# Optimization experiments

Measured on AMD Instinct MI355X. Metric: run time of the kernel, lower is better.

The kernel has to match this reference:

```python
import jax, jax.numpy as jnp
from jax import lax
import numpy as np

EPS = 1e-5
DN = ('NCHW', 'OIHW', 'NCHW')


def conv_s2(x, w):
    # Conv2d k=4 s=2 p=1, no bias
    return lax.conv_general_dilated(x, w, (2, 2), [(1, 1), (1, 1)], dimension_numbers=DN)


def deconv_s2(x, w):
    # ConvTranspose2d k=4 s=2 p=1; torch weight layout (in, out, kH, kW)
    w_ = jnp.flip(w, (2, 3)).transpose(1, 0, 2, 3)  # -> (out, in, kH, kW)
    return lax.conv_general_dilated(x, w_, (1, 1), [(2, 2), (2, 2)],
                                    lhs_dilation=(2, 2), dimension_numbers=DN)


def bn_train(x, gamma, beta):
    # BatchNorm2d in training mode: batch stats over (N, H, W), biased variance
    m = jnp.mean(x, axis=(0, 2, 3), keepdims=True)
    v = jnp.var(x, axis=(0, 2, 3), keepdims=True)
    g = gamma.reshape(1, -1, 1, 1)
    b = beta.reshape(1, -1, 1, 1)
    return (x - m) * jax.lax.rsqrt(v + EPS) * g + b


def lrelu(x):
    return jnp.where(x >= 0, x, 0.2 * x)


def setup_inputs() -> dict:
    key = jax.random.key(0)
    ks = jax.random.split(key, 32)
    nef = 64
    d = {}
    d['x'] = jax.random.normal(ks[0], (256, 3, 64, 64), dtype=jnp.float32)
    # encoder conv weights (O, I, 4, 4), init N(0, 0.02)
    d['w1'] = 0.02 * jax.random.normal(ks[1], (nef, 3, 4, 4), jnp.float32)
    d['w2'] = 0.02 * jax.random.normal(ks[2], (nef * 2, nef, 4, 4), jnp.float32)
    d['w3'] = 0.02 * jax.random.normal(ks[3], (nef * 4, nef * 2, 4, 4), jnp.float32)
    d['w4'] = 0.02 * jax.random.normal(ks[4], (nef * 8, nef * 4, 4, 4), jnp.float32)
    # bn params: weight ~ N(1, 0.02), bias = 0
    for i, c in enumerate([nef, nef * 2, nef * 4, nef * 8]):
        d[f'g{i+1}'] = 1.0 + 0.02 * jax.random.normal(ks[5 + i], (c,), jnp.float32)
        d[f'b{i+1}'] = jnp.zeros((c,), jnp.float32)
    # 512 channel-wise Linear(16,16): torch default init U(-1/4, 1/4)
    bound = 1.0 / 4.0
    d['cw_w'] = jax.random.uniform(ks[9], (512, 16, 16), jnp.float32, -bound, bound)
    d['cw_b'] = jax.random.uniform(ks[10], (512, 16), jnp.float32, -bound, bound)
    # decoder deconv weights in torch layout (in, out, 4, 4)
    d['dw1'] = 0.02 * jax.random.normal(ks[11], (nef * 8, nef * 4, 4, 4), jnp.float32)
    d['dw2'] = 0.02 * jax.random.normal(ks[12], (nef * 4, nef * 2, 4, 4), jnp.float32)
    d['dw3'] = 0.02 * jax.random.normal(ks[13], (nef * 2, nef, 4, 4), jnp.float32)
    d['dw4'] = 0.02 * jax.random.normal(ks[14], (nef, 3, 4, 4), jnp.float32)
    for i, c in enumerate([nef * 4, nef * 2, nef]):
        d[f'dg{i+1}'] = 1.0 + 0.02 * jax.random.normal(ks[15 + i], (c,), jnp.float32)
        d[f'db{i+1}'] = jnp.zeros((c,), jnp.float32)
    return d


def reference(x, w1, w2, w3, w4, g1, b1, g2, b2, g3, b3, g4, b4,
              cw_w, cw_b, dw1, dw2, dw3, dw4, dg1, db1, dg2, db2, dg3, db3):
    h = lrelu(bn_train(conv_s2(x, w1), g1, b1))
    h = lrelu(bn_train(conv_s2(h, w2), g2, b2))
    h = lrelu(bn_train(conv_s2(h, w3), g3, b3))
    h = lrelu(bn_train(conv_s2(h, w4), g4, b4))  # (B, 512, 4, 4)
    B, C, H, W = h.shape
    flat = h.reshape(B, C, H * W)  # (B, 512, 16)
    # per-channel Linear: y[b,c,t] = sum_s flat[b,c,s] * cw_w[c,t,s] + cw_b[c,t]
    flat = jnp.einsum('bcs,cts->bct', flat, cw_w) + cw_b[None, :, :]
    h = flat.reshape(B, C, H, W)
    h = jax.nn.relu(bn_train(deconv_s2(h, dw1), dg1, db1))
    h = jax.nn.relu(bn_train(deconv_s2(h, dw2), dg2, db2))
    h = jax.nn.relu(bn_train(deconv_s2(h, dw3), dg3, db3))
    return jnp.tanh(deconv_s2(h, dw4))
```

## Files before the change

### kernel.cpp

```cpp
#include <hip/hip_runtime.h>
#include <math.h>

typedef _Float16 f16;
typedef __attribute__((ext_vector_type(8))) _Float16 f16x8;
typedef __attribute__((ext_vector_type(16))) float f32x16;

union U64x2 { unsigned long long u[2]; f16x8 v; };
union Q16   { uint4 q; unsigned long long u[2]; };

constexpr int ilog2c(int x) { return x <= 1 ? 0 : 1 + ilog2c(x >> 1); }

__device__ __forceinline__ float fast_tanh(float x) {
    float e = __expf(2.f * x);
    return (e - 1.f) / (e + 1.f);
}

template<int CIN,int IH,int IW,int OH,int OW,int COUT,int COB,int SPT,int KS,
         int CO_FR,bool DEC>
__global__ __launch_bounds__(256,2) void mfma_conv(
    const f16* __restrict__ xin, const f16* __restrict__ wp,
    f16* __restrict__ out16, float* __restrict__ out32, size_t ps,
    float* __restrict__ psumF, float* __restrict__ psqF)
{
    constexpr int OHo  = DEC ? OH/2 : OH;
    constexpr int OWo  = DEC ? OW/2 : OW;
    constexpr int KTOT = CIN * (DEC ? 4 : 16);
    constexpr int CH   = (KTOT/64) / KS;
    constexpr int RPT  = CIN / 64;
    constexpr int RSH  = (RPT==1?0:RPT==2?1:RPT==4?2:3);
    constexpr int WSTR = CIN * 16;
    constexpr int TPR  = 256 / COB;
    constexpr int NU4  = 8 / TPR;
    constexpr int SPB  = OHo * OWo;
    constexpr int LSPB = ilog2c(SPB);
    constexpr int LOWo = ilog2c(OWo);

    __shared__ unsigned long long Xs[SPT*17];
    __shared__ unsigned long long Wls[COB*17];

    const int t   = threadIdx.x;
    const int bx  = blockIdx.x;
    const int cob = blockIdx.y;
    const int bz  = blockIdx.z;
    const int par = DEC ? (bz & 3) : 0;
    const int ks  = DEC ? (bz >> 2) : bz;
    const int poh = par >> 1, pw = par & 1;

    const int gsp_s = bx*SPT + t;
    const int img_s = gsp_s >> LSPB;
    const int r_s   = gsp_s & (SPB-1);
    const int oy_s  = r_s >> LOWo;
    const int ox_s  = r_s & (OWo-1);

    const int wco   = t / TPR;
    const int wpart = t % TPR;
    const f16* wbase = wp + (size_t)(cob*COB + wco)*WSTR + wpart*(64/TPR);

    const int wave = t >> 6, lane = t & 63, half = lane >> 5, l31 = lane & 31;
    const int co_w = (wave >> 1) * (CO_FR*32);
    const int sp_w = (wave & 1) * 128;

    f32x16 acc[CO_FR][4];
    #pragma unroll
    for (int i = 0; i < CO_FR; ++i)
        #pragma unroll
        for (int b = 0; b < 4; ++b)
            #pragma unroll
            for (int r = 0; r < 16; ++r) acc[i][b][r] = 0.f;

    uint4 xreg[8];
    uint4 wreg[NU4];

    auto issue = [&](int cc) {
        const int gc  = ks*CH + cc;
        const int tap = gc >> RSH;
        const int ci0 = (gc & (RPT-1)) << 6;
        int kh, kw, ih, iw;
        if (DEC) {
            const int t2h = tap >> 1, t2w = tap & 1;
            kh = (1-poh) + 2*t2h; kw = (1-pw) + 2*t2w;
            ih = oy_s + poh - t2h; iw = ox_s + pw - t2w;
        } else {
            kh = tap >> 2; kw = tap & 3;
            ih = 2*oy_s - 1 + kh; iw = 2*ox_s - 1 + kw;
        }
        const int woff = (kh*4 + kw)*CIN + ci0;
        const uint4* wsrc = (const uint4*)(wbase + woff);
        #pragma unroll
        for (int j = 0; j < NU4; ++j) wreg[j] = wsrc[j];
        const bool ok = (unsigned)ih < (unsigned)IH && (unsigned)iw < (unsigned)IW;
        if (ok) {
            const uint4* xsrc = (const uint4*)
                (xin + ((size_t)(img_s*IH + ih)*IW + iw)*CIN + ci0);
            #pragma unroll
            for (int j = 0; j < 8; ++j) xreg[j] = xsrc[j];
        } else {
            #pragma unroll
            for (int j = 0; j < 8; ++j) xreg[j] = uint4{0u,0u,0u,0u};
        }
    };

    issue(0);

    for (int cc = 0; cc < CH; ++cc) {
        if (cc) __syncthreads();

        #pragma unroll
        for (int j = 0; j < NU4; ++j) {
            Q16 v; v.q = wreg[j];
            const int u0 = wco*17 + wpart*(NU4*2) + j*2;
            Wls[u0]   = v.u[0];
            Wls[u0+1] = v.u[1];
        }
        {
            const int u0 = t*17;
            #pragma unroll
            for (int j = 0; j < 8; ++j) {
                Q16 v; v.q = xreg[j];
                Xs[u0 + j*2]   = v.u[0];
                Xs[u0 + j*2+1] = v.u[1];
            }
        }

        if (cc + 1 < CH) issue(cc + 1);

        asm volatile("s_waitcnt lgkmcnt(0)" ::: "memory");
        __builtin_amdgcn_sched_barrier(0);
        __builtin_amdgcn_s_barrier();
        __builtin_amdgcn_sched_barrier(0);

        #pragma unroll
        for (int kk = 0; kk < 4; ++kk) {
            const int uo = kk*4 + 2*half;
            f16x8 wf[CO_FR], xf[4];
            #pragma unroll
            for (int i = 0; i < CO_FR; ++i) {
                U64x2 u; const int rw = (co_w + i*32 + l31)*17 + uo;
                u.u[0] = Wls[rw]; u.u[1] = Wls[rw+1]; wf[i] = u.v;
            }
            #pragma unroll
            for (int b = 0; b < 4; ++b) {
                U64x2 u; const int rx = (sp_w + b*32 + l31)*17 + uo;
                u.u[0] = Xs[rx]; u.u[1] = Xs[rx+1]; xf[b] = u.v;
            }
            #pragma unroll
            for (int i = 0; i < CO_FR; ++i)
                #pragma unroll
                for (int b = 0; b < 4; ++b)
                    acc[i][b] = __builtin_amdgcn_mfma_f32_32x32x16_f16(
                        xf[b], wf[i], acc[i][b], 0, 0, 0);
        }
    }

    #pragma unroll
    for (int b = 0; b < 4; ++b) {
        #pragma unroll
        for (int q = 0; q < 4; ++q) {
            #pragma unroll
            for (int r2 = 0; r2 < 4; ++r2) {
                const int sp_loc = sp_w + b*32 + q*8 + 4*half + r2;
                const int gsp    = bx*SPT + sp_loc;
                size_t base;
                if (DEC) {
                    const int img = gsp >> LSPB;
                    const int r   = gsp & (SPB-1);
                    const int oh  = 2*(r >> LOWo) + poh;
                    const int ow  = 2*(r & (OWo-1)) + pw;
                    base = ((size_t)(img*OH + oh)*OW + ow)*COUT + cob*COB;
                } else {
                    base = (size_t)gsp*COUT + cob*COB;
                }
                #pragma unroll
                for (int i = 0; i < CO_FR; ++i) {
                    const int co_l = co_w + i*32 + l31;
                    const float v  = acc[i][b][q*4 + r2];
                    if (KS == 1) out16[base + co_l] = (_Float16)v;
                    else         out32[(size_t)ks*ps + base + co_l] = v;
                }
            }
        }
    }

    if (KS == 1 && psumF != nullptr) {
        #pragma unroll
        for (int i = 0; i < CO_FR; ++i) {
            float s = 0.f, q = 0.f;
            #pragma unroll
            for (int b = 0; b < 4; ++b)
                #pragma unroll
                for (int r = 0; r < 16; ++r) {
                    const float v = acc[i][b][r];
                    s += v; q += v * v;
                }
            s += __shfl_down(s, 32);
            q += __shfl_down(q, 32);
            if (half == 0) {
                const int co = cob*COB + co_w + i*32 + l31;
                atomicAdd(psumF + co, s);
                atomicAdd(psqF + co, q);
            }
        }
    }
}

__global__ __launch_bounds__(256,2) void conv1_mfma(
    const f16* __restrict__ xp, const f16* __restrict__ wp,
    f16* __restrict__ out, float* __restrict__ psumF, float* __restrict__ psqF)
{
    __shared__ unsigned long long Xs[256*17];
    __shared__ unsigned long long Wls[64*17];
    const int t = threadIdx.x, bx = blockIdx.x;

    {
        const int r = t >> 2, part = t & 3;
        const uint4* src = (const uint4*)(wp + r*64 + part*16);
        Q16 v0; v0.q = src[0];
        Q16 v1; v1.q = src[1];
        const int u0 = r*17 + part*4;
        Wls[u0]   = v0.u[0]; Wls[u0+1] = v0.u[1];
        Wls[u0+2] = v1.u[0]; Wls[u0+3] = v1.u[1];
    }
    {
        const int gsp = bx*256 + t;
        const int n = gsp >> 10, r = gsp & 1023;
        const int oy = r >> 5, ox = r & 31;
        const int ih0 = 2*oy - 1, iw0 = 2*ox - 1;
        const int u0 = t*17;
        #pragma unroll
        for (int tap = 0; tap < 16; ++tap) {
            const int ih = ih0 + (tap >> 2), iw = iw0 + (tap & 3);
            unsigned long long v = 0ull;
            if ((unsigned)ih < 64u && (unsigned)iw < 64u)
                v = *(const unsigned long long*)(xp + (((size_t)n*64 + ih)*64 + iw)*4);
            Xs[u0 + tap] = v;
        }
    }
    __syncthreads();

    const int wave = t >> 6, lane = t & 63, half = lane >> 5, l31 = lane & 31;
    const int co_w = (wave >> 1) * 32;
    const int sp_w = (wave & 1) * 128;

    f32x16 acc[4];
    #pragma unroll
    for (int b = 0; b < 4; ++b)
        #pragma unroll
        for (int r = 0; r < 16; ++r) acc[b][r] = 0.f;

    #pragma unroll
    for (int kk = 0; kk < 4; ++kk) {
        const int uo = kk*4 + 2*half;
        U64x2 uw; const int rw = (co_w + l31)*17 + uo;
        uw.u[0] = Wls[rw]; uw.u[1] = Wls[rw+1];
        #pragma unroll
        for (int b = 0; b < 4; ++b) {
            U64x2 ux; const int rx = (sp_w + b*32 + l31)*17 + uo;
            ux.u[0] = Xs[rx]; ux.u[1] = Xs[rx+1];
            acc[b] = __builtin_amdgcn_mfma_f32_32x32x16_f16(
                ux.v, uw.v, acc[b], 0, 0, 0);
        }
    }
    #pragma unroll
    for (int b = 0; b < 4; ++b)
        #pragma unroll
        for (int q = 0; q < 4; ++q)
            #pragma unroll
            for (int r2 = 0; r2 < 4; ++r2) {
                const int sp_loc = sp_w + b*32 + q*8 + 4*half + r2;
                out[(size_t)(bx*256 + sp_loc)*64 + co_w + l31] =
                    (_Float16)acc[b][q*4 + r2];
            }

    float s = 0.f, q = 0.f;
    #pragma unroll
    for (int b = 0; b < 4; ++b)
        #pragma unroll
        for (int r = 0; r < 16; ++r) {
            const float v = acc[b][r];
            s += v; q += v * v;
        }
    s += __shfl_down(s, 32);
    q += __shfl_down(q, 32);
    if (half == 0) {
        const int co = co_w + l31;
        atomicAdd(psumF + co, s);
        atomicAdd(psqF + co, q);
    }
}

__global__ __launch_bounds__(256,2) void deconv4_mfma(
    const f16* __restrict__ xin, const f16* __restrict__ wp,
    float* __restrict__ out)
{
    __shared__ unsigned long long Xs[256*17];
    __shared__ unsigned long long Wls[32*17];

    const int t   = threadIdx.x;
    const int bx  = blockIdx.x;
    const int par = blockIdx.y;
    const int poh = par >> 1, pw = par & 1;

    const int gsp_s = bx*256 + t;
    const int img_s = gsp_s >> 10;
    const int r_s   = gsp_s & 1023;
    const int oy_s  = r_s >> 5;
    const int ox_s  = r_s & 31;

    const int wco   = t >> 3;
    const int wpart = t & 7;

    const int wave = t >> 6, lane = t & 63, half = lane >> 5, l31 = lane & 31;
    const int sp_w = wave * 64;

    f32x16 acc[2];
    #pragma unroll
    for (int b = 0; b < 2; ++b)
        #pragma unroll
        for (int r = 0; r < 16; ++r) acc[b][r] = 0.f;

    uint4 xreg[8];
    uint4 wreg1;

    auto issue4 = [&](int cc) {
        const int t2h = cc >> 1, t2w = cc & 1;
        const int kh = (1-poh) + 2*t2h, kw = (1-pw) + 2*t2w;
        const int ih = oy_s + poh - t2h, iw = ox_s + pw - t2w;
        wreg1 = *(const uint4*)(wp + wco*1024 + (kh*4 + kw)*64 + wpart*8);
        const bool ok = (unsigned)ih < 32u && (unsigned)iw < 32u;
        if (ok) {
            const uint4* src = (const uint4*)
                (xin + ((size_t)(img_s*32 + ih)*32 + iw)*64);
            #pragma unroll
            for (int j = 0; j < 8; ++j) xreg[j] = src[j];
        } else {
            #pragma unroll
            for (int j = 0; j < 8; ++j) xreg[j] = uint4{0u,0u,0u,0u};
        }
    };

    issue4(0);

    for (int cc = 0; cc < 4; ++cc) {
        if (cc) __syncthreads();
        {
            Q16 v; v.q = wreg1;
            const int u0 = wco*17 + wpart*2;
            Wls[u0] = v.u[0]; Wls[u0+1] = v.u[1];
        }
        {
            const int u0 = t*17;
            #pragma unroll
            for (int j = 0; j < 8; ++j) {
                Q16 v; v.q = xreg[j];
                Xs[u0 + j*2]   = v.u[0];
                Xs[u0 + j*2+1] = v.u[1];
            }
        }
        if (cc + 1 < 4) issue4(cc + 1);
        asm volatile("s_waitcnt lgkmcnt(0)" ::: "memory");
        __builtin_amdgcn_sched_barrier(0);
        __builtin_amdgcn_s_barrier();
        __builtin_amdgcn_sched_barrier(0);

        #pragma unroll
        for (int kk = 0; kk < 4; ++kk) {
            const int uo = kk*4 + 2*half;
            U64x2 uw; const int rw = l31*17 + uo;
            uw.u[0] = Wls[rw]; uw.u[1] = Wls[rw+1];
            #pragma unroll
            for (int b = 0; b < 2; ++b) {
                U64x2 ux; const int rx = (sp_w + b*32 + l31)*17 + uo;
                ux.u[0] = Xs[rx]; ux.u[1] = Xs[rx+1];
                acc[b] = __builtin_amdgcn_mfma_f32_32x32x16_f16(
                    uw.v, ux.v, acc[b], 0, 0, 0);
            }
        }
    }

    if (half == 0) {
        #pragma unroll
        for (int b = 0; b < 2; ++b) {
            const int gsp = bx*256 + sp_w + b*32 + l31;
            const int img = gsp >> 10;
            const int r   = gsp & 1023;
            const int oh  = 2*(r >> 5) + poh;
            const int ow  = 2*(r & 31) + pw;
            #pragma unroll
            for (int co = 0; co < 3; ++co)
                out[(((size_t)img*3 + co)*64 + oh)*64 + ow] =
                    fast_tanh(acc[b][co]);
        }
    }
}

__global__ __launch_bounds__(256) void prep_x(
    const float* __restrict__ x, f16* __restrict__ xp)
{
    const int i = blockIdx.x*256 + threadIdx.x;
    const int n = i >> 12, p = i & 4095;
    const float* b = x + (size_t)n*12288 + p;
    union { _Float16 h[4]; unsigned long long u; } o;
    o.h[0] = (_Float16)b[0];
    o.h[1] = (_Float16)b[4096];
    o.h[2] = (_Float16)b[8192];
    o.h[3] = (_Float16)0.f;
    *(unsigned long long*)(xp + (size_t)i*4) = o.u;
}

__global__ __launch_bounds__(256) void prep_w1(
    const float* __restrict__ w1, f16* __restrict__ wp)
{
    const int e = blockIdx.x*256 + threadIdx.x;
    const int co = e >> 6, k = e & 63, tap = k >> 2, ci = k & 3;
    const float v = (ci < 3) ? w1[(co*3 + ci)*16 + tap] : 0.f;
    wp[e] = (_Float16)v;
}

__global__ __launch_bounds__(256) void prep_w4(
    const float* __restrict__ dw4, f16* __restrict__ wp)
{
    const int e = blockIdx.x*256 + threadIdx.x;
    const int co = e >> 10, r = e & 1023, khw = r >> 6, ci = r & 63;
    const float v = (co < 3) ? dw4[(ci*3 + co)*16 + khw] : 0.f;
    wp[e] = (_Float16)v;
}

__global__ __launch_bounds__(256) void prep_w(
    const float* __restrict__ w2, const float* __restrict__ w3,
    const float* __restrict__ w4, const float* __restrict__ dw1,
    const float* __restrict__ dw2, const float* __restrict__ dw3,
    f16* __restrict__ dst)
{
    const int e = blockIdx.x*256 + threadIdx.x;
    float v;
    if (e < 131072) {
        int co = e >> 10, r = e & 1023, khw = r >> 6, ci = r & 63;
        v = w2[(co*64 + ci)*16 + khw];
    } else if (e < 655360) {
        int l = e - 131072;
        int co = l >> 11, r = l & 2047, khw = r >> 7, ci = r & 127;
        v = w3[(co*128 + ci)*16 + khw];
    } else if (e < 2752512) {
        int l = e - 655360;
        int co = l >> 12, r = l & 4095, khw = r >> 8, ci = r & 255;
        v = w4[(co*256 + ci)*16 + khw];
    } else if (e < 4849664) {
        int l = e - 2752512;
        int co = l >> 13, r = l & 8191, khw = r >> 9, ci = r & 511;
        v = dw1[(ci*256 + co)*16 + khw];
    } else if (e < 5373952) {
        int l = e - 4849664;
        int co = l >> 12, r = l & 4095, khw = r >> 8, ci = r & 255;
        v = dw2[(ci*128 + co)*16 + khw];
    } else {
        int l = e - 5373952;
        int co = l >> 11, r = l & 2047, khw = r >> 7, ci = r & 127;
        v = dw3[(ci*64 + co)*16 + khw];
    }
    dst[e] = (_Float16)v;
}

template<typename T, int P>
__global__ __launch_bounds__(256) void bn_partial(
    const T* __restrict__ x, size_t ps, float* __restrict__ psum,
    float* __restrict__ psq, int C, int rowsPerS, int S)
{
    const int s = blockIdx.x;
    const int c = (blockIdx.y << 6) + (threadIdx.x & 63);
    float a = 0.f, q = 0.f;
    const int rEnd = (s + 1) * rowsPerS;
    for (int r = s*rowsPerS + (threadIdx.x >> 6); r < rEnd; r += 4) {
        float v = 0.f;
        #pragma unroll
        for (int p = 0; p < P; ++p)
            v += (float)x[p*ps + (size_t)r * C + c];
        a += v; q += v * v;
    }
    __shared__ float ls[256], lq[256];
    ls[threadIdx.x] = a; lq[threadIdx.x] = q;
    __syncthreads();
    if (threadIdx.x < 64) {
        a = ls[threadIdx.x] + ls[threadIdx.x+64] + ls[threadIdx.x+128] + ls[threadIdx.x+192];
        q = lq[threadIdx.x] + lq[threadIdx.x+64] + lq[threadIdx.x+128] + lq[threadIdx.x+192];
        psum[c * S + s] = a; psq[c * S + s] = q;
    }
}

__global__ __launch_bounds__(256) void bn_finalize(
    const float* __restrict__ psum, const float* __restrict__ psq,
    const float* __restrict__ gamma, const float* __restrict__ beta,
    float* __restrict__ scale, float* __restrict__ shift,
    int C, int S, float inv_count)
{
    int c = blockIdx.x * 256 + threadIdx.x;
    if (c >= C) return;
    float s = 0.f, q = 0.f;
    for (int i = 0; i < S; ++i) { s += psum[c*S + i]; q += psq[c*S + i]; }
    float m   = s * inv_count;
    float var = q * inv_count - m * m;
    var = var < 0.f ? 0.f : var;
    float sc = gamma[c] * rsqrtf(var + 1e-5f);
    scale[c] = sc;
    shift[c] = beta[c] - m * sc;
}

__global__ __launch_bounds__(256) void bn_act16f(
    f16* __restrict__ x, const float* __restrict__ psum, const float* __restrict__ psq,
    const float* __restrict__ gamma, const float* __restrict__ beta,
    int Cmask, float inv_count, float slope)
{
    const size_t i8 = ((size_t)blockIdx.x*256 + threadIdx.x) * 8;
    union { uint4 u; _Float16 h[8]; } a;
    a.u = *(const uint4*)(x + i8);
    const int c0 = (int)(i8 & (size_t)Cmask);
    #pragma unroll
    for (int j = 0; j < 8; ++j) {
        const int c = c0 + j;
        float m   = psum[c] * inv_count;
        float var = psq[c] * inv_count - m * m;
        var = var < 0.f ? 0.f : var;
        float sc = gamma[c] * rsqrtf(var + 1e-5f);
        float sh = beta[c] - m * sc;
        float v = (float)a.h[j] * sc + sh;
        a.h[j] = (_Float16)(v >= 0.f ? v : slope * v);
    }
    *(uint4*)(x + i8) = a.u;
}

template<int P>
__global__ __launch_bounds__(256) void bn_act32(
    const float* __restrict__ x, size_t ps, f16* __restrict__ y,
    const float* __restrict__ sc, const float* __restrict__ sh,
    int Cmask, float slope)
{
    const size_t i8 = ((size_t)blockIdx.x*256 + threadIdx.x) * 8;
    float xv[8] = {0,0,0,0,0,0,0,0};
    #pragma unroll
    for (int p = 0; p < P; ++p) {
        float4 v0 = *(const float4*)(x + p*ps + i8);
        float4 v1 = *(const float4*)(x + p*ps + i8 + 4);
        xv[0]+=v0.x; xv[1]+=v0.y; xv[2]+=v0.z; xv[3]+=v0.w;
        xv[4]+=v1.x; xv[5]+=v1.y; xv[6]+=v1.z; xv[7]+=v1.w;
    }
    union { uint4 u; _Float16 h[8]; } a;
    const int c0 = (int)(i8 & (size_t)Cmask);
    #pragma unroll
    for (int j = 0; j < 8; ++j) {
        float v = xv[j] * sc[c0+j] + sh[c0+j];
        a.h[j] = (_Float16)(v >= 0.f ? v : slope * v);
    }
    *(uint4*)(y + i8) = a.u;
}

__global__ __launch_bounds__(256) void chanlin16(
    const f16* __restrict__ in, const float* __restrict__ w,
    const float* __restrict__ bias, f16* __restrict__ out)
{
    const int i = blockIdx.x*256 + threadIdx.x;
    const int c  = i & 511;
    const int bt = i >> 9;
    const int b  = bt >> 4, tt = bt & 15;
    const f16* src = in + ((size_t)b*16)*512 + c;
    const float* wr = w + ((size_t)c*16 + tt)*16;
    float acc = bias[c*16 + tt];
    #pragma unroll
    for (int s = 0; s < 16; ++s)
        acc = fmaf((float)src[s*512], wr[s], acc);
    out[i] = (_Float16)acc;
}

extern "C" void kernel_launch(void* const* d_in, const int* in_sizes, int n_in,
                              void* d_out, int out_size, void* d_ws, size_t ws_size,
                              hipStream_t stream)
{
    const float* x   = (const float*)d_in[0];
    const float* w1  = (const float*)d_in[1];
    const float* w2  = (const float*)d_in[2];
    const float* w3  = (const float*)d_in[3];
    const float* w4  = (const float*)d_in[4];
    const float* g1  = (const float*)d_in[5];
    const float* b1  = (const float*)d_in[6];
    const float* g2  = (const float*)d_in[7];
    const float* b2  = (const float*)d_in[8];
    const float* g3  = (const float*)d_in[9];
    const float* b3  = (const float*)d_in[10];
    const float* g4  = (const float*)d_in[11];
    const float* b4  = (const float*)d_in[12];
    const float* cww = (const float*)d_in[13];
    const float* cwb = (const float*)d_in[14];
    const float* dw1 = (const float*)d_in[15];
    const float* dw2 = (const float*)d_in[16];
    const float* dw3 = (const float*)d_in[17];
    const float* dw4 = (const float*)d_in[18];
    const float* dg1 = (const float*)d_in[19];
    const float* db1 = (const float*)d_in[20];
    const float* dg2 = (const float*)d_in[21];
    const float* db2 = (const float*)d_in[22];
    const float* dg3 = (const float*)d_in[23];
    const float* db3 = (const float*)d_in[24];

    char* WS = (char*)d_ws;
    float* psum  = (float*)WS;
    float* psq   = (float*)(WS + 65536);
    float* scale = (float*)(WS + 131072);
    float* shift = (float*)(WS + 133120);
    float* fst   = (float*)(WS + 196608);
    f16* slotA   = (f16*)(WS + 262144);
    f16* slotB   = (f16*)(WS + 262144 + 33554432);
    f16* wprep   = (f16*)(WS + 84148224);
    f16* wprep1  = wprep + 5505024;
    f16* wprep4  = wprep1 + 4096;

    f16*   A_hi  = slotA + 8388608;
    float* pB    = (float*)slotB;
    f16*   xpack = slotA;

    float* fs0 = fst;          float* fs1 = fst + 1024;
    float* fs2 = fst + 2048;   float* fs4 = fst + 4096;
    float* fs5 = fst + 5120;   float* fs6 = fst + 6144;

    hipMemsetAsync(fst, 0, 28672, stream);
    prep_w<<<21504, 256, 0, stream>>>(w2, w3, w4, dw1, dw2, dw3, wprep);
    prep_w1<<<16, 256, 0, stream>>>(w1, wprep1);
    prep_w4<<<128, 256, 0, stream>>>(dw4, wprep4);
    prep_x<<<4096, 256, 0, stream>>>(x, xpack);

    conv1_mfma<<<1024, 256, 0, stream>>>(xpack, wprep1, slotB, fs0, fs0 + 512);
    bn_act16f<<<8192, 256, 0, stream>>>(slotB, fs0, fs0 + 512, g1, b1, 63, 1.f/262144.f, 0.2f);

    mfma_conv<64,32,32,16,16,128, 128,256,1,2,false><<<dim3(256,1,1), 256, 0, stream>>>(
        slotB, wprep, slotA, nullptr, 0, fs1, fs1 + 512);
    bn_act16f<<<4096, 256, 0, stream>>>(slotA, fs1, fs1 + 512, g2, b2, 127, 1.f/65536.f, 0.2f);

    mfma_conv<128,16,16,8,8,256, 64,256,1,1,false><<<dim3(64,4,1), 256, 0, stream>>>(
        slotA, wprep + 131072, A_hi, nullptr, 0, fs2, fs2 + 512);
    bn_act16f<<<2048, 256, 0, stream>>>(A_hi, fs2, fs2 + 512, g3, b3, 255, 1.f/16384.f, 0.2f);

    mfma_conv<256,8,8,4,4,512, 128,256,4,2,false><<<dim3(16,4,4), 256, 0, stream>>>(
        A_hi, wprep + 655360, nullptr, pB, (size_t)2097152, nullptr, nullptr);
    bn_partial<float,4><<<dim3(32,8), 256, 0, stream>>>(pB, (size_t)2097152, psum, psq, 512, 128, 32);
    bn_finalize<<<2, 256, 0, stream>>>(psum, psq, g4, b4, scale, shift, 512, 32, 1.f/4096.f);
    bn_act32<4><<<1024, 256, 0, stream>>>(pB, (size_t)2097152, slotA, scale, shift, 511, 0.2f);

    chanlin16<<<8192, 256, 0, stream>>>(slotA, cww, cwb, slotB);

    mfma_conv<512,4,4,8,8,256, 64,256,1,1,true><<<dim3(16,4,4), 256, 0, stream>>>(
        slotB, wprep + 2752512, A_hi, nullptr, 0, fs4, fs4 + 512);
    bn_act16f<<<2048, 256, 0, stream>>>(A_hi, fs4, fs4 + 512, dg1, db1, 255, 1.f/16384.f, 0.f);

    mfma_conv<256,8,8,16,16,128, 128,256,1,2,true><<<dim3(64,1,4), 256, 0, stream>>>(
        A_hi, wprep + 4849664, slotB, nullptr, 0, fs5, fs5 + 512);
    bn_act16f<<<4096, 256, 0, stream>>>(slotB, fs5, fs5 + 512, dg2, db2, 127, 1.f/65536.f, 0.f);

    mfma_conv<128,16,16,32,32,64, 64,256,1,1,true><<<dim3(256,1,4), 256, 0, stream>>>(
        slotB, wprep + 5373952, slotA, nullptr, 0, fs6, fs6 + 512);
    bn_act16f<<<8192, 256, 0, stream>>>(slotA, fs6, fs6 + 512, dg3, db3, 63, 1.f/262144.f, 0.f);

    deconv4_mfma<<<dim3(1024,4), 256, 0, stream>>>(slotA, wprep4, (float*)d_out);
}
```

Measured before the change: 613.7 us.

## Load weight fragments directly from global into registers and double-buffer input LDS

Weight MFMA fragments are now read by each lane straight from global memory into registers, dropping the weight shared-memory staging. The input tile in LDS is double-buffered, which lets the leading __syncthreads per chunk be removed. The aim is to cut LDS traffic and one barrier per K-chunk. In exchange it doubles the input LDS footprint, adds register pressure from the weight fragments, and makes weight loads exposed with no prefetch because they are issued in the same iteration they are used.

```diff
diff --git a/kernel.cpp b/kernel.cpp
--- a/kernel.cpp
+++ b/kernel.cpp
@@ -7,6 +7,7 @@
 
 union U64x2 { unsigned long long u[2]; f16x8 v; };
 union Q16   { uint4 q; unsigned long long u[2]; };
+union UW    { uint4 q; f16x8 v; };
 
 constexpr int ilog2c(int x) { return x <= 1 ? 0 : 1 + ilog2c(x >> 1); }
 
@@ -29,14 +30,11 @@
     constexpr int RPT  = CIN / 64;
     constexpr int RSH  = (RPT==1?0:RPT==2?1:RPT==4?2:3);
     constexpr int WSTR = CIN * 16;
-    constexpr int TPR  = 256 / COB;
-    constexpr int NU4  = 8 / TPR;
     constexpr int SPB  = OHo * OWo;
     constexpr int LSPB = ilog2c(SPB);
     constexpr int LOWo = ilog2c(OWo);
 
-    __shared__ unsigned long long Xs[SPT*17];
-    __shared__ unsigned long long Wls[COB*17];
+    __shared__ unsigned long long Xs[2][SPT*17];
 
     const int t   = threadIdx.x;
     const int bx  = blockIdx.x;
@@ -52,14 +50,15 @@
     const int oy_s  = r_s >> LOWo;
     const int ox_s  = r_s & (OWo-1);
 
-    const int wco   = t / TPR;
-    const int wpart = t % TPR;
-    const f16* wbase = wp + (size_t)(cob*COB + wco)*WSTR + wpart*(64/TPR);
-
     const int wave = t >> 6, lane = t & 63, half = lane >> 5, l31 = lane & 31;
     const int co_w = (wave >> 1) * (CO_FR*32);
     const int sp_w = (wave & 1) * 128;
 
+    const f16* wrow[CO_FR];
+    #pragma unroll
+    for (int i = 0; i < CO_FR; ++i)
+        wrow[i] = wp + (size_t)(cob*COB + co_w + i*32 + l31)*WSTR + 8*half;
+
     f32x16 acc[CO_FR][4];
     #pragma unroll
     for (int i = 0; i < CO_FR; ++i)
@@ -69,25 +68,19 @@
             for (int r = 0; r < 16; ++r) acc[i][b][r] = 0.f;
 
     uint4 xreg[8];
-    uint4 wreg[NU4];
-
-    auto issue = [&](int cc) {
+    uint4 wfrag[CO_FR][4];
+
+    auto issueX = [&](int cc) {
         const int gc  = ks*CH + cc;
         const int tap = gc >> RSH;
         const int ci0 = (gc & (RPT-1)) << 6;
-        int kh, kw, ih, iw;
+        int ih, iw;
         if (DEC) {
             const int t2h = tap >> 1, t2w = tap & 1;
-            kh = (1-poh) + 2*t2h; kw = (1-pw) + 2*t2w;
             ih = oy_s + poh - t2h; iw = ox_s + pw - t2w;
         } else {
-            kh = tap >> 2; kw = tap & 3;
-            ih = 2*oy_s - 1 + kh; iw = 2*ox_s - 1 + kw;
-        }
-        const int woff = (kh*4 + kw)*CIN + ci0;
-        const uint4* wsrc = (const uint4*)(wbase + woff);
-        #pragma unroll
-        for (int j = 0; j < NU4; ++j) wreg[j] = wsrc[j];
+            ih = 2*oy_s - 1 + (tap >> 2); iw = 2*ox_s - 1 + (tap & 3);
+        }
         const bool ok = (unsigned)ih < (unsigned)IH && (unsigned)iw < (unsigned)IW;
         if (ok) {
             const uint4* xsrc = (const uint4*)
@@ -100,29 +93,42 @@
         }
     };
 
-    issue(0);
+    auto loadW = [&](int cc) {
+        const int gc  = ks*CH + cc;
+        const int tap = gc >> RSH;
+        const int ci0 = (gc & (RPT-1)) << 6;
+        int kh, kw;
+        if (DEC) {
+            kh = (1-poh) + 2*(tap >> 1); kw = (1-pw) + 2*(tap & 1);
+        } else {
+            kh = tap >> 2; kw = tap & 3;
+        }
+        const int woff = (kh*4 + kw)*CIN + ci0;
+        #pragma unroll
+        for (int i = 0; i < CO_FR; ++i)
+            #pragma unroll
+            for (int kk = 0; kk < 4; ++kk)
+                wfrag[i][kk] = *(const uint4*)(wrow[i] + woff + kk*16);
+    };
+
+    issueX(0);
 
     for (int cc = 0; cc < CH; ++cc) {
-        if (cc) __syncthreads();
-
-        #pragma unroll
-        for (int j = 0; j < NU4; ++j) {
-            Q16 v; v.q = wreg[j];
-            const int u0 = wco*17 + wpart*(NU4*2) + j*2;
-            Wls[u0]   = v.u[0];
-            Wls[u0+1] = v.u[1];
-        }
+        const int buf = cc & 1;
+
+        loadW(cc);
+
         {
             const int u0 = t*17;
             #pragma unroll
             for (int j = 0; j < 8; ++j) {
                 Q16 v; v.q = xreg[j];
-                Xs[u0 + j*2]   = v.u[0];
-                Xs[u0 + j*2+1] = v.u[1];
-            }
-        }
-
-        if (cc + 1 < CH) issue(cc + 1);
+                Xs[buf][u0 + j*2]   = v.u[0];
+                Xs[buf][u0 + j*2+1] = v.u[1];
+            }
+        }
+
+        if (cc + 1 < CH) issueX(cc + 1);
 
         asm volatile("s_waitcnt lgkmcnt(0)" ::: "memory");
         __builtin_amdgcn_sched_barrier(0);
@@ -135,13 +141,12 @@
             f16x8 wf[CO_FR], xf[4];
             #pragma unroll
             for (int i = 0; i < CO_FR; ++i) {
-                U64x2 u; const int rw = (co_w + i*32 + l31)*17 + uo;
-                u.u[0] = Wls[rw]; u.u[1] = Wls[rw+1]; wf[i] = u.v;
+                UW u; u.q = wfrag[i][kk]; wf[i] = u.v;
             }
             #pragma unroll
             for (int b = 0; b < 4; ++b) {
                 U64x2 u; const int rx = (sp_w + b*32 + l31)*17 + uo;
-                u.u[0] = Xs[rx]; u.u[1] = Xs[rx+1]; xf[b] = u.v;
+                u.u[0] = Xs[buf][rx]; u.u[1] = Xs[buf][rx+1]; xf[b] = u.v;
             }
             #pragma unroll
             for (int i = 0; i < CO_FR; ++i)
@@ -292,8 +297,7 @@
     const f16* __restrict__ xin, const f16* __restrict__ wp,
     float* __restrict__ out)
 {
-    __shared__ unsigned long long Xs[256*17];
-    __shared__ unsigned long long Wls[32*17];
+    __shared__ unsigned long long Xs[2][256*17];
 
     const int t   = threadIdx.x;
     const int bx  = blockIdx.x;
@@ -306,12 +310,11 @@
     const int oy_s  = r_s >> 5;
     const int ox_s  = r_s & 31;
 
-    const int wco   = t >> 3;
-    const int wpart = t & 7;
-
     const int wave = t >> 6, lane = t & 63, half = lane >> 5, l31 = lane & 31;
     const int sp_w = wave * 64;
 
+    const f16* wrow = wp + l31*1024 + 8*half;
+
     f32x16 acc[2];
     #pragma unroll
     for (int b = 0; b < 2; ++b)
@@ -319,13 +322,11 @@
         for (int r = 0; r < 16; ++r) acc[b][r] = 0.f;
 
     uint4 xreg[8];
-    uint4 wreg1;
-
-    auto issue4 = [&](int cc) {
+    uint4 wfrag[4];
+
+    auto issueX4 = [&](int cc) {
         const int t2h = cc >> 1, t2w = cc & 1;
-        const int kh = (1-poh) + 2*t2h, kw = (1-pw) + 2*t2w;
         const int ih = oy_s + poh - t2h, iw = ox_s + pw - t2w;
-        wreg1 = *(const uint4*)(wp + wco*1024 + (kh*4 + kw)*64 + wpart*8);
         const bool ok = (unsigned)ih < 32u && (unsigned)iw < 32u;
         if (ok) {
             const uint4* src = (const uint4*)
@@ -338,25 +339,30 @@
         }
     };
 
-    issue4(0);
+    auto loadW4 = [&](int cc) {
+        const int t2h = cc >> 1, t2w = cc & 1;
+        const int kh = (1-poh) + 2*t2h, kw = (1-pw) + 2*t2w;
+        const int woff = (kh*4 + kw)*64;
+        #pragma unroll
+        for (int kk = 0; kk < 4; ++kk)
+            wfrag[kk] = *(const uint4*)(wrow + woff + kk*16);
+    };
+
+    issueX4(0);
 
     for (int cc = 0; cc < 4; ++cc) {
-        if (cc) __syncthreads();
-        {
-            Q16 v; v.q = wreg1;
-            const int u0 = wco*17 + wpart*2;
-            Wls[u0] = v.u[0]; Wls[u0+1] = v.u[1];
-        }
+        const int buf = cc & 1;
+        loadW4(cc);
         {
             const int u0 = t*17;
             #pragma unroll
             for (int j = 0; j < 8; ++j) {
                 Q16 v; v.q = xreg[j];
-                Xs[u0 + j*2]   = v.u[0];
-                Xs[u0 + j*2+1] = v.u[1];
-            }
-        }
-        if (cc + 1 < 4) issue4(cc + 1);
+                Xs[buf][u0 + j*2]   = v.u[0];
+                Xs[buf][u0 + j*2+1] = v.u[1];
+            }
+        }
+        if (cc + 1 < 4) issueX4(cc + 1);
         asm volatile("s_waitcnt lgkmcnt(0)" ::: "memory");
         __builtin_amdgcn_sched_barrier(0);
         __builtin_amdgcn_s_barrier();
@@ -365,12 +371,11 @@
         #pragma unroll
         for (int kk = 0; kk < 4; ++kk) {
             const int uo = kk*4 + 2*half;
-            U64x2 uw; const int rw = l31*17 + uo;
-            uw.u[0] = Wls[rw]; uw.u[1] = Wls[rw+1];
+            UW uw; uw.q = wfrag[kk];
             #pragma unroll
             for (int b = 0; b < 2; ++b) {
                 U64x2 ux; const int rx = (sp_w + b*32 + l31)*17 + uo;
-                ux.u[0] = Xs[rx]; ux.u[1] = Xs[rx+1];
+                ux.u[0] = Xs[buf][rx]; ux.u[1] = Xs[buf][rx+1];
                 acc[b] = __builtin_amdgcn_mfma_f32_32x32x16_f16(
                     uw.v, ux.v, acc[b], 0, 0, 0);
             }
```

After: 692.6 us. 1.13x slower.

## Coalesce activation loads across threads, add XCD block swizzle, pair-unroll K loop

Applied to the files above, without the earlier changes.

Global activation loads are restructured so that 8 consecutive threads read one spatial position's 64-channel row, each taking a 16-byte slice, rather than each thread reading a full 128-byte row alone. This makes accesses coalesced across neighbouring lanes. Block indices are remapped so that consecutive tiles land on the same XCD, which is meant to improve L2 locality. The K loop is unrolled in pairs with ping-pong weight registers. The trade-off is more per-load address arithmetic and bounds checks, and higher register pressure.

```diff
diff --git a/kernel.cpp b/kernel.cpp
--- a/kernel.cpp
+++ b/kernel.cpp
@@ -13,6 +13,10 @@
 __device__ __forceinline__ float fast_tanh(float x) {
     float e = __expf(2.f * x);
     return (e - 1.f) / (e + 1.f);
+}
+
+__device__ __forceinline__ int xcd_swz(int bx, int n) {
+    return ((n & 7) == 0) ? ((bx & 7) * (n >> 3) + (bx >> 3)) : bx;
 }
 
 template<int CIN,int IH,int IW,int OH,int OW,int COUT,int COB,int SPT,int KS,
@@ -34,23 +38,22 @@
     constexpr int SPB  = OHo * OWo;
     constexpr int LSPB = ilog2c(SPB);
     constexpr int LOWo = ilog2c(OWo);
+    static_assert(CH % 2 == 0, "pair-unrolled K loop needs even CH");
 
     __shared__ unsigned long long Xs[SPT*17];
     __shared__ unsigned long long Wls[COB*17];
 
     const int t   = threadIdx.x;
-    const int bx  = blockIdx.x;
+    const int bx  = xcd_swz(blockIdx.x, gridDim.x);
     const int cob = blockIdx.y;
     const int bz  = blockIdx.z;
     const int par = DEC ? (bz & 3) : 0;
     const int ks  = DEC ? (bz >> 2) : bz;
     const int poh = par >> 1, pw = par & 1;
 
-    const int gsp_s = bx*SPT + t;
-    const int img_s = gsp_s >> LSPB;
-    const int r_s   = gsp_s & (SPB-1);
-    const int oy_s  = r_s >> LOWo;
-    const int ox_s  = r_s & (OWo-1);
+    const int rloc  = t >> 3;
+    const int sub8  = (t & 7) * 8;
+    const int gbase = bx*SPT + rloc;
 
     const int wco   = t / TPR;
     const int wpart = t % TPR;
@@ -69,60 +72,66 @@
             for (int r = 0; r < 16; ++r) acc[i][b][r] = 0.f;
 
     uint4 xreg[8];
-    uint4 wreg[NU4];
-
-    auto issue = [&](int cc) {
+    uint4 wregA[NU4], wregB[NU4];
+
+    auto issueX = [&](int cc) {
         const int gc  = ks*CH + cc;
         const int tap = gc >> RSH;
         const int ci0 = (gc & (RPT-1)) << 6;
-        int kh, kw, ih, iw;
-        if (DEC) {
-            const int t2h = tap >> 1, t2w = tap & 1;
-            kh = (1-poh) + 2*t2h; kw = (1-pw) + 2*t2w;
-            ih = oy_s + poh - t2h; iw = ox_s + pw - t2w;
-        } else {
-            kh = tap >> 2; kw = tap & 3;
-            ih = 2*oy_s - 1 + kh; iw = 2*ox_s - 1 + kw;
-        }
+        int dh, dw;
+        if (DEC) { dh = poh - (tap >> 1); dw = pw - (tap & 1); }
+        else     { dh = (tap >> 2) - 1;   dw = (tap & 3) - 1; }
+        #pragma unroll
+        for (int j = 0; j < 8; ++j) {
+            const int gsp = gbase + j*32;
+            const int img = gsp >> LSPB;
+            const int rr  = gsp & (SPB-1);
+            const int oy  = rr >> LOWo;
+            const int ox  = rr & (OWo-1);
+            const int ih  = (DEC ? oy : 2*oy) + dh;
+            const int iw  = (DEC ? ox : 2*ox) + dw;
+            const bool ok = (unsigned)ih < (unsigned)IH && (unsigned)iw < (unsigned)IW;
+            if (ok) {
+                xreg[j] = *(const uint4*)
+                    (xin + ((size_t)(img*IH + ih)*IW + iw)*CIN + ci0 + sub8);
+            } else {
+                xreg[j] = uint4{0u,0u,0u,0u};
+            }
+        }
+    };
+
+    auto issueW = [&](int cc, uint4 (&wr)[NU4]) {
+        const int gc  = ks*CH + cc;
+        const int tap = gc >> RSH;
+        const int ci0 = (gc & (RPT-1)) << 6;
+        int kh, kw;
+        if (DEC) { kh = (1-poh) + 2*(tap >> 1); kw = (1-pw) + 2*(tap & 1); }
+        else     { kh = tap >> 2;               kw = tap & 3; }
         const int woff = (kh*4 + kw)*CIN + ci0;
         const uint4* wsrc = (const uint4*)(wbase + woff);
         #pragma unroll
-        for (int j = 0; j < NU4; ++j) wreg[j] = wsrc[j];
-        const bool ok = (unsigned)ih < (unsigned)IH && (unsigned)iw < (unsigned)IW;
-        if (ok) {
-            const uint4* xsrc = (const uint4*)
-                (xin + ((size_t)(img_s*IH + ih)*IW + iw)*CIN + ci0);
-            #pragma unroll
-            for (int j = 0; j < 8; ++j) xreg[j] = xsrc[j];
-        } else {
-            #pragma unroll
-            for (int j = 0; j < 8; ++j) xreg[j] = uint4{0u,0u,0u,0u};
-        }
+        for (int j = 0; j < NU4; ++j) wr[j] = wsrc[j];
     };
 
-    issue(0);
-
-    for (int cc = 0; cc < CH; ++cc) {
+    auto body = [&](int cc, uint4 (&wcur)[NU4], uint4 (&wnext)[NU4], bool more) {
         if (cc) __syncthreads();
 
         #pragma unroll
+        for (int j = 0; j < 8; ++j) {
+            Q16 v; v.q = xreg[j];
+            const int u0 = (rloc + j*32)*17 + (sub8 >> 2);
+            Xs[u0]   = v.u[0];
+            Xs[u0+1] = v.u[1];
+        }
+        #pragma unroll
         for (int j = 0; j < NU4; ++j) {
-            Q16 v; v.q = wreg[j];
+            Q16 v; v.q = wcur[j];
             const int u0 = wco*17 + wpart*(NU4*2) + j*2;
             Wls[u0]   = v.u[0];
             Wls[u0+1] = v.u[1];
         }
-        {
-            const int u0 = t*17;
-            #pragma unroll
-            for (int j = 0; j < 8; ++j) {
-                Q16 v; v.q = xreg[j];
-                Xs[u0 + j*2]   = v.u[0];
-                Xs[u0 + j*2+1] = v.u[1];
-            }
-        }
-
-        if (cc + 1 < CH) issue(cc + 1);
+
+        if (more) { issueX(cc + 1); issueW(cc + 1, wnext); }
 
         asm volatile("s_waitcnt lgkmcnt(0)" ::: "memory");
         __builtin_amdgcn_sched_barrier(0);
@@ -150,6 +159,13 @@
                     acc[i][b] = __builtin_amdgcn_mfma_f32_32x32x16_f16(
                         xf[b], wf[i], acc[i][b], 0, 0, 0);
         }
+    };
+
+    issueX(0);
+    issueW(0, wregA);
+    for (int cc = 0; cc < CH; cc += 2) {
+        body(cc,   wregA, wregB, true);
+        body(cc+1, wregB, wregA, cc+2 < CH);
     }
 
     #pragma unroll
@@ -209,7 +225,8 @@
 {
     __shared__ unsigned long long Xs[256*17];
     __shared__ unsigned long long Wls[64*17];
-    const int t = threadIdx.x, bx = blockIdx.x;
+    const int t = threadIdx.x;
+    const int bx = xcd_swz(blockIdx.x, gridDim.x);
 
     {
         const int r = t >> 2, part = t & 3;
@@ -296,15 +313,13 @@
     __shared__ unsigned long long Wls[32*17];
 
     const int t   = threadIdx.x;
-    const int bx  = blockIdx.x;
+    const int bx  = xcd_swz(blockIdx.x, gridDim.x);
     const int par = blockIdx.y;
     const int poh = par >> 1, pw = par & 1;
 
-    const int gsp_s = bx*256 + t;
-    const int img_s = gsp_s >> 10;
-    const int r_s   = gsp_s & 1023;
-    const int oy_s  = r_s >> 5;
-    const int ox_s  = r_s & 31;
+    const int rloc  = t >> 3;
+    const int sub8  = (t & 7) * 8;
+    const int gbase = bx*256 + rloc;
 
     const int wco   = t >> 3;
     const int wpart = t & 7;
@@ -319,44 +334,48 @@
         for (int r = 0; r < 16; ++r) acc[b][r] = 0.f;
 
     uint4 xreg[8];
-    uint4 wreg1;
-
-    auto issue4 = [&](int cc) {
-        const int t2h = cc >> 1, t2w = cc & 1;
-        const int kh = (1-poh) + 2*t2h, kw = (1-pw) + 2*t2w;
-        const int ih = oy_s + poh - t2h, iw = ox_s + pw - t2w;
-        wreg1 = *(const uint4*)(wp + wco*1024 + (kh*4 + kw)*64 + wpart*8);
-        const bool ok = (unsigned)ih < 32u && (unsigned)iw < 32u;
-        if (ok) {
-            const uint4* src = (const uint4*)
-                (xin + ((size_t)(img_s*32 + ih)*32 + iw)*64);
-            #pragma unroll
-            for (int j = 0; j < 8; ++j) xreg[j] = src[j];
-        } else {
-            #pragma unroll
-            for (int j = 0; j < 8; ++j) xreg[j] = uint4{0u,0u,0u,0u};
+    uint4 wregA, wregB;
+
+    auto issueX4 = [&](int cc) {
+        const int dh = poh - (cc >> 1), dw = pw - (cc & 1);
+        #pragma unroll
+        for (int j = 0; j < 8; ++j) {
+            const int gsp = gbase + j*32;
+            const int img = gsp >> 10;
+            const int rr  = gsp & 1023;
+            const int oy  = rr >> 5;
+            const int ox  = rr & 31;
+            const int ih  = oy + dh, iw = ox + dw;
+            const bool ok = (unsigned)ih < 32u && (unsigned)iw < 32u;
+            if (ok) {
+                xreg[j] = *(const uint4*)
+                    (xin + ((size_t)(img*32 + ih)*32 + iw)*64 + sub8);
+            } else {
+                xreg[j] = uint4{0u,0u,0u,0u};
+            }
         }
     };
 
-    issue4(0);
-
-    for (int cc = 0; cc < 4; ++cc) {
+    auto issueW4 = [&](int cc, uint4& wr) {
+        const int kh = (1-poh) + 2*(cc >> 1), kw = (1-pw) + 2*(cc & 1);
+        wr = *(const uint4*)(wp + wco*1024 + (kh*4 + kw)*64 + wpart*8);
+    };
+
+    auto body4 = [&](int cc, uint4& wcur, uint4& wnext, bool more) {
         if (cc) __syncthreads();
+        #pragma unroll
+        for (int j = 0; j < 8; ++j) {
+            Q16 v; v.q = xreg[j];
+            const int u0 = (rloc + j*32)*17 + (sub8 >> 2);
+            Xs[u0]   = v.u[0];
+            Xs[u0+1] = v.u[1];
+        }
         {
-            Q16 v; v.q = wreg1;
+            Q16 v; v.q = wcur;
             const int u0 = wco*17 + wpart*2;
             Wls[u0] = v.u[0]; Wls[u0+1] = v.u[1];
         }
-        {
-            const int u0 = t*17;
-            #pragma unroll
-            for (int j = 0; j < 8; ++j) {
-                Q16 v; v.q = xreg[j];
-                Xs[u0 + j*2]   = v.u[0];
-                Xs[u0 + j*2+1] = v.u[1];
-            }
-        }
-        if (cc + 1 < 4) issue4(cc + 1);
+        if (more) { issueX4(cc + 1); issueW4(cc + 1, wnext); }
         asm volatile("s_waitcnt lgkmcnt(0)" ::: "memory");
         __builtin_amdgcn_sched_barrier(0);
         __builtin_amdgcn_s_barrier();
@@ -375,7 +394,14 @@
                     uw.v, ux.v, acc[b], 0, 0, 0);
             }
         }
-    }
+    };
+
+    issueX4(0);
+    issueW4(0, wregA);
+    body4(0, wregA, wregB, true);
+    body4(1, wregB, wregA, true);
+    body4(2, wregA, wregB, true);
+    body4(3, wregB, wregA, false);
 
     if (half == 0) {
         #pragma unroll
```

After: 689.1 us. 12.3% more time.

## XOR-swizzle LDS tiles, raise occupancy, and halve output-channel tiles

Applied to the files above, without the earlier changes.

Replaces the padded stride-17 LDS layout with a stride-16 layout that XOR-swizzles the 16-byte chunks by row, so each ds read stays 16-byte aligned and avoids bank conflicts. It raises the launch-bounds minimum blocks from 2 to 4 in the MFMA conv kernels. Three conv launches move from COB=128 with CO_FR=2 to COB=64 with CO_FR=1, doubling the grid. More blocks and fewer accumulators per block should help latency hiding, but each block reuses its loaded input tile across fewer output channels, and the tighter register budget could cause spills.

```diff
diff --git a/kernel.cpp b/kernel.cpp
--- a/kernel.cpp
+++ b/kernel.cpp
@@ -17,7 +17,7 @@
 
 template<int CIN,int IH,int IW,int OH,int OW,int COUT,int COB,int SPT,int KS,
          int CO_FR,bool DEC>
-__global__ __launch_bounds__(256,2) void mfma_conv(
+__global__ __launch_bounds__(256,4) void mfma_conv(
     const f16* __restrict__ xin, const f16* __restrict__ wp,
     f16* __restrict__ out16, float* __restrict__ out32, size_t ps,
     float* __restrict__ psumF, float* __restrict__ psqF)
@@ -35,8 +35,8 @@
     constexpr int LSPB = ilog2c(SPB);
     constexpr int LOWo = ilog2c(OWo);
 
-    __shared__ unsigned long long Xs[SPT*17];
-    __shared__ unsigned long long Wls[COB*17];
+    __shared__ unsigned long long Xs[SPT*16];
+    __shared__ unsigned long long Wls[COB*16];
 
     const int t   = threadIdx.x;
     const int bx  = blockIdx.x;
@@ -59,6 +59,7 @@
     const int wave = t >> 6, lane = t & 63, half = lane >> 5, l31 = lane & 31;
     const int co_w = (wave >> 1) * (CO_FR*32);
     const int sp_w = (wave & 1) * 128;
+    const int swz  = l31 & 7;
 
     f32x16 acc[CO_FR][4];
     #pragma unroll
@@ -108,17 +109,18 @@
         #pragma unroll
         for (int j = 0; j < NU4; ++j) {
             Q16 v; v.q = wreg[j];
-            const int u0 = wco*17 + wpart*(NU4*2) + j*2;
+            const int sl = wpart*NU4 + j;
+            const int u0 = wco*16 + ((sl ^ (wco & 7)) << 1);
             Wls[u0]   = v.u[0];
             Wls[u0+1] = v.u[1];
         }
         {
-            const int u0 = t*17;
             #pragma unroll
             for (int j = 0; j < 8; ++j) {
                 Q16 v; v.q = xreg[j];
-                Xs[u0 + j*2]   = v.u[0];
-                Xs[u0 + j*2+1] = v.u[1];
+                const int u0 = t*16 + ((j ^ (t & 7)) << 1);
+                Xs[u0]   = v.u[0];
+                Xs[u0+1] = v.u[1];
             }
         }
 
@@ -131,16 +133,16 @@
 
         #pragma unroll
         for (int kk = 0; kk < 4; ++kk) {
-            const int uo = kk*4 + 2*half;
+            const int so = ((kk*2 + half) ^ swz) << 1;
             f16x8 wf[CO_FR], xf[4];
             #pragma unroll
             for (int i = 0; i < CO_FR; ++i) {
-                U64x2 u; const int rw = (co_w + i*32 + l31)*17 + uo;
+                U64x2 u; const int rw = (co_w + i*32 + l31)*16 + so;
                 u.u[0] = Wls[rw]; u.u[1] = Wls[rw+1]; wf[i] = u.v;
             }
             #pragma unroll
             for (int b = 0; b < 4; ++b) {
-                U64x2 u; const int rx = (sp_w + b*32 + l31)*17 + uo;
+                U64x2 u; const int rx = (sp_w + b*32 + l31)*16 + so;
                 u.u[0] = Xs[rx]; u.u[1] = Xs[rx+1]; xf[b] = u.v;
             }
             #pragma unroll
@@ -203,12 +205,12 @@
     }
 }
 
-__global__ __launch_bounds__(256,2) void conv1_mfma(
+__global__ __launch_bounds__(256,4) void conv1_mfma(
     const f16* __restrict__ xp, const f16* __restrict__ wp,
     f16* __restrict__ out, float* __restrict__ psumF, float* __restrict__ psqF)
 {
-    __shared__ unsigned long long Xs[256*17];
-    __shared__ unsigned long long Wls[64*17];
+    __shared__ unsigned long long Xs[256*16];
+    __shared__ unsigned long long Wls[64*16];
     const int t = threadIdx.x, bx = blockIdx.x;
 
     {
@@ -216,23 +218,24 @@
         const uint4* src = (const uint4*)(wp + r*64 + part*16);
         Q16 v0; v0.q = src[0];
         Q16 v1; v1.q = src[1];
-        const int u0 = r*17 + part*4;
-        Wls[u0]   = v0.u[0]; Wls[u0+1] = v0.u[1];
-        Wls[u0+2] = v1.u[0]; Wls[u0+3] = v1.u[1];
+        const int a0 = r*16 + (((part*2)   ^ (r & 7)) << 1);
+        const int a1 = r*16 + (((part*2+1) ^ (r & 7)) << 1);
+        Wls[a0]   = v0.u[0]; Wls[a0+1] = v0.u[1];
+        Wls[a1]   = v1.u[0]; Wls[a1+1] = v1.u[1];
     }
     {
         const int gsp = bx*256 + t;
         const int n = gsp >> 10, r = gsp & 1023;
         const int oy = r >> 5, ox = r & 31;
         const int ih0 = 2*oy - 1, iw0 = 2*ox - 1;
-        const int u0 = t*17;
         #pragma unroll
         for (int tap = 0; tap < 16; ++tap) {
             const int ih = ih0 + (tap >> 2), iw = iw0 + (tap & 3);
             unsigned long long v = 0ull;
             if ((unsigned)ih < 64u && (unsigned)iw < 64u)
                 v = *(const unsigned long long*)(xp + (((size_t)n*64 + ih)*64 + iw)*4);
-            Xs[u0 + tap] = v;
+            const int u = t*16 + (((tap >> 1) ^ (t & 7)) << 1) + (tap & 1);
+            Xs[u] = v;
         }
     }
     __syncthreads();
@@ -240,6 +243,7 @@
     const int wave = t >> 6, lane = t & 63, half = lane >> 5, l31 = lane & 31;
     const int co_w = (wave >> 1) * 32;
     const int sp_w = (wave & 1) * 128;
+    const int swz  = l31 & 7;
 
     f32x16 acc[4];
     #pragma unroll
@@ -249,12 +253,12 @@
 
     #pragma unroll
     for (int kk = 0; kk < 4; ++kk) {
-        const int uo = kk*4 + 2*half;
-        U64x2 uw; const int rw = (co_w + l31)*17 + uo;
+        const int so = ((kk*2 + half) ^ swz) << 1;
+        U64x2 uw; const int rw = (co_w + l31)*16 + so;
         uw.u[0] = Wls[rw]; uw.u[1] = Wls[rw+1];
         #pragma unroll
         for (int b = 0; b < 4; ++b) {
-            U64x2 ux; const int rx = (sp_w + b*32 + l31)*17 + uo;
+            U64x2 ux; const int rx = (sp_w + b*32 + l31)*16 + so;
             ux.u[0] = Xs[rx]; ux.u[1] = Xs[rx+1];
             acc[b] = __builtin_amdgcn_mfma_f32_32x32x16_f16(
                 ux.v, uw.v, acc[b], 0, 0, 0);
@@ -288,12 +292,12 @@
     }
 }
 
-__global__ __launch_bounds__(256,2) void deconv4_mfma(
+__global__ __launch_bounds__(256,4) void deconv4_mfma(
     const f16* __restrict__ xin, const f16* __restrict__ wp,
     float* __restrict__ out)
 {
-    __shared__ unsigned long long Xs[256*17];
-    __shared__ unsigned long long Wls[32*17];
+    __shared__ unsigned long long Xs[256*16];
+    __shared__ unsigned long long Wls[32*16];
 
     const int t   = threadIdx.x;
     const int bx  = blockIdx.x;
@@ -311,6 +315,7 @@
 
     const int wave = t >> 6, lane = t & 63, half = lane >> 5, l31 = lane & 31;
     const int sp_w = wave * 64;
+    const int swz  = l31 & 7;
 
     f32x16 acc[2];
     #pragma unroll
@@ -344,16 +349,16 @@
         if (cc) __syncthreads();
         {
             Q16 v; v.q = wreg1;
-            const int u0 = wco*17 + wpart*2;
+            const int u0 = wco*16 + ((wpart ^ (wco & 7)) << 1);
             Wls[u0] = v.u[0]; Wls[u0+1] = v.u[1];
         }
         {
-            const int u0 = t*17;
             #pragma unroll
             for (int j = 0; j < 8; ++j) {
                 Q16 v; v.q = xreg[j];
-                Xs[u0 + j*2]   = v.u[0];
-                Xs[u0 + j*2+1] = v.u[1];
+                const int u0 = t*16 + ((j ^ (t & 7)) << 1);
+                Xs[u0]   = v.u[0];
+                Xs[u0+1] = v.u[1];
             }
         }
         if (cc + 1 < 4) issue4(cc + 1);
@@ -364,12 +369,12 @@
 
         #pragma unroll
         for (int kk = 0; kk < 4; ++kk) {
-            const int uo = kk*4 + 2*half;
-            U64x2 uw; const int rw = l31*17 + uo;
+            const int so = ((kk*2 + half) ^ swz) << 1;
+            U64x2 uw; const int rw = l31*16 + so;
             uw.u[0] = Wls[rw]; uw.u[1] = Wls[rw+1];
             #pragma unroll
             for (int b = 0; b < 2; ++b) {
-                U64x2 ux; const int rx = (sp_w + b*32 + l31)*17 + uo;
+                U64x2 ux; const int rx = (sp_w + b*32 + l31)*16 + so;
                 ux.u[0] = Xs[rx]; ux.u[1] = Xs[rx+1];
                 acc[b] = __builtin_amdgcn_mfma_f32_32x32x16_f16(
                     uw.v, ux.v, acc[b], 0, 0, 0);
@@ -628,7 +633,7 @@
     conv1_mfma<<<1024, 256, 0, stream>>>(xpack, wprep1, slotB, fs0, fs0 + 512);
     bn_act16f<<<8192, 256, 0, stream>>>(slotB, fs0, fs0 + 512, g1, b1, 63, 1.f/262144.f, 0.2f);
 
-    mfma_conv<64,32,32,16,16,128, 128,256,1,2,false><<<dim3(256,1,1), 256, 0, stream>>>(
+    mfma_conv<64,32,32,16,16,128, 64,256,1,1,false><<<dim3(256,2,1), 256, 0, stream>>>(
         slotB, wprep, slotA, nullptr, 0, fs1, fs1 + 512);
     bn_act16f<<<4096, 256, 0, stream>>>(slotA, fs1, fs1 + 512, g2, b2, 127, 1.f/65536.f, 0.2f);
 
@@ -636,7 +641,7 @@
         slotA, wprep + 131072, A_hi, nullptr, 0, fs2, fs2 + 512);
     bn_act16f<<<2048, 256, 0, stream>>>(A_hi, fs2, fs2 + 512, g3, b3, 255, 1.f/16384.f, 0.2f);
 
-    mfma_conv<256,8,8,4,4,512, 128,256,4,2,false><<<dim3(16,4,4), 256, 0, stream>>>(
+    mfma_conv<256,8,8,4,4,512, 64,256,4,1,false><<<dim3(16,8,4), 256, 0, stream>>>(
         A_hi, wprep + 655360, nullptr, pB, (size_t)2097152, nullptr, nullptr);
     bn_partial<float,4><<<dim3(32,8), 256, 0, stream>>>(pB, (size_t)2097152, psum, psq, 512, 128, 32);
     bn_finalize<<<2, 256, 0, stream>>>(psum, psq, g4, b4, scale, shift, 512, 32, 1.f/4096.f);
@@ -648,7 +653,7 @@
         slotB, wprep + 2752512, A_hi, nullptr, 0, fs4, fs4 + 512);
     bn_act16f<<<2048, 256, 0, stream>>>(A_hi, fs4, fs4 + 512, dg1, db1, 255, 1.f/16384.f, 0.f);
 
-    mfma_conv<256,8,8,16,16,128, 128,256,1,2,true><<<dim3(64,1,4), 256, 0, stream>>>(
+    mfma_conv<256,8,8,16,16,128, 64,256,1,1,true><<<dim3(64,2,4), 256, 0, stream>>>(
         A_hi, wprep + 4849664, slotB, nullptr, 0, fs5, fs5 + 512);
     bn_act16f<<<4096, 256, 0, stream>>>(slotB, fs5, fs5 + 512, dg2, db2, 127, 1.f/65536.f, 0.f);
 
```

After: 894.3 us. 45.7% more time.
